# Optimization experiments

Measured on AMD Instinct MI355X. Metric: run time of the kernel, lower is better.

Reference implementation:

```python
import jax, jax.numpy as jnp
import numpy as np

TEMPERATURE = 1.0
# softmax over 32768 db entries gives mean score ~3e-5; threshold 5e-5 makes the
# mask non-trivial (torch default threshold=0.0 would keep everything).
THRESHOLD = 5e-5


def setup_inputs() -> dict:
    key = jax.random.key(0)
    kq, kd = jax.random.split(key)
    queries = jax.random.normal(kq, (8192, 512), dtype=jnp.float32)
    db = jax.random.normal(kd, (32768, 512), dtype=jnp.float32)
    return {"queries": queries, "db": db, "k": 20}


def reference(queries, db, k):
    # similarity matmul: [Nq, Ndb]
    sim_mat = (queries @ db.T) / TEMPERATURE
    # torch does .float().softmax(dim=1)
    all_scores = jax.nn.softmax(sim_mat.astype(jnp.float32), axis=1)
    # db is provided explicitly -> mask_diag = False; k = min(k, db_size)
    k = min(k, db.shape[0])
    topk_scores, topk_inds = jax.lax.top_k(all_scores, k)  # sorted=True
    mask = topk_scores > THRESHOLD
    n_retrieved_per_query = mask.sum(axis=1)
    # padded equivalent of the nonzero-gather: below-threshold slots zeroed
    retrieved_scores = jnp.where(mask, topk_scores, 0.0)
    return retrieved_scores, topk_inds, n_retrieved_per_query, mask
```

## Files before the change

### kernel.cpp

```cpp
#include <hip/hip_runtime.h>
#include <hip/hip_bf16.h>
#include <float.h>
#include <limits.h>

#define NQ 8192
#define ND 32768
#define KD 512
#define TOPK 20
#define NCAND 32
#define NS 16
#define SLICE 2048
#define SEMIT 24
#define EBASE 64.0f
#define ALPHA 2.75f
#define NT (SLICE / 128 * 8)

typedef _Float16 f16x8 __attribute__((ext_vector_type(8)));
typedef _Float16 f16x4 __attribute__((ext_vector_type(4)));
typedef __fp16   hp16x2 __attribute__((ext_vector_type(2)));
typedef float    f32x4 __attribute__((ext_vector_type(4)));

#define CSW(a, b) { unsigned mx_ = (a) > (b) ? (a) : (b); \
                    unsigned mn_ = (a) > (b) ? (b) : (a); (a) = mx_; (b) = mn_; }

__device__ __forceinline__ float fexp64(float q) {
  return __builtin_amdgcn_exp2f(__builtin_fmaf(q, 1.44269504f,
                                               -EBASE * 1.44269504f));
}

__global__ __launch_bounds__(256) void tohalf(
    const float* __restrict__ src, _Float16* __restrict__ dst, int n4)
{
  int g = blockIdx.x * 256 + threadIdx.x;
  if (g >= n4) return;
  float4 v = ((const float4*)src)[g];
  f16x4 h = {(_Float16)v.x, (_Float16)v.y, (_Float16)v.z, (_Float16)v.w};
  ((f16x4*)dst)[g] = h;
}

__device__ __forceinline__ void gload16(const _Float16* g, _Float16* l) {
  __builtin_amdgcn_global_load_lds(
      (const __attribute__((address_space(1))) unsigned int*)g,
      (__attribute__((address_space(3))) unsigned int*)l, 16, 0, 0);
}

#define INSL(x) if ((x) > L7) { L7 = (x); \
  CSW(L6, L7); CSW(L5, L6); CSW(L4, L5); CSW(L3, L4); \
  CSW(L2, L3); CSW(L1, L2); CSW(L0, L1); }
#define INSM(x) if ((x) > M7) { M7 = (x); \
  CSW(M6, M7); CSW(M5, M6); CSW(M4, M5); CSW(M3, M4); \
  CSW(M2, M3); CSW(M1, M2); CSW(M0, M1); }

#define EPIPAIR(va, vb, c0, ES, INS, T) { \
  if (fmaxf((va), (vb)) > (T)) { \
    hp16x2 hp_ = __builtin_amdgcn_cvt_pkrtz((va), (vb)); \
    unsigned pk_ = __builtin_bit_cast(unsigned, hp_); \
    ES += fexp64((float)hp_[0]); \
    ES += fexp64((float)hp_[1]); \
    unsigned sg_ = (pk_ >> 15) & 0x10001u; \
    unsigned u2_ = pk_ ^ (0x80008000u ^ (sg_ * 0x7FFFu)); \
    unsigned k0_ = (u2_ << 16) | (unsigned)(c0); \
    unsigned k1_ = (u2_ & 0xFFFF0000u) | (unsigned)((c0) - 1); \
    INS(k0_); INS(k1_); } }

__global__ __launch_bounds__(256, 2) void fusedsel(
    const _Float16* __restrict__ Qh, const _Float16* __restrict__ Dh,
    unsigned* __restrict__ scand, float* __restrict__ ssum)
{
  __shared__ _Float16 Bs[3][128 * 64];

  const int t = threadIdx.x;
  const int w = t >> 6, l = t & 63;
  const int m0 = blockIdx.x * 128;
  const int ns = blockIdx.y;
  const int lane_mn = l & 15, quad = l >> 4;
  const int row0 = m0 + w * 32 + lane_mn;
  const int row1 = row0 + 16;

  const int sRowIn = l >> 3;
  const int sq = (l & 7) ^ (sRowIn & 7);
  const int fs0 = quad ^ (lane_mn & 7);
  const int fs1 = fs0 ^ 4;

  f16x8 af0[16], af1[16];
  #pragma unroll
  for (int i = 0; i < 16; i++) {
    af0[i] = *(const f16x8*)(Qh + (size_t)row0 * KD + i * 32 + quad * 8);
    af1[i] = *(const f16x8*)(Qh + (size_t)row1 * KD + i * 32 + quad * 8);
  }

  #pragma unroll
  for (int j = 0; j < 4; j++)
    gload16(Dh + (size_t)(ns * SLICE + w * 8 + j * 32 + sRowIn) * KD + sq * 8,
            &Bs[0][(w * 8 + j * 32) * 64]);
  #pragma unroll
  for (int j = 0; j < 4; j++)
    gload16(Dh + (size_t)(ns * SLICE + w * 8 + j * 32 + sRowIn) * KD + 64 + sq * 8,
            &Bs[1][(w * 8 + j * 32) * 64]);

  float nq0 = 0.f, nq1 = 0.f;
  #pragma unroll
  for (int i = 0; i < 16; i++) {
    #pragma unroll
    for (int e = 0; e < 8; e++) {
      float a0 = (float)af0[i][e], a1 = (float)af1[i][e];
      nq0 = __builtin_fmaf(a0, a0, nq0);
      nq1 = __builtin_fmaf(a1, a1, nq1);
    }
  }
  nq0 += __shfl_xor(nq0, 16); nq0 += __shfl_xor(nq0, 32);
  nq1 += __shfl_xor(nq1, 16); nq1 += __shfl_xor(nq1, 32);
  const float T0 = ALPHA * __builtin_sqrtf(nq0);
  const float T1 = ALPHA * __builtin_sqrtf(nq1);

  unsigned L0=0,L1=0,L2=0,L3=0,L4=0,L5=0,L6=0,L7=0;
  unsigned M0=0,M1=0,M2=0,M3=0,M4=0,M5=0,M6=0,M7=0;
  float es0 = 0.f, es1 = 0.f;

  asm volatile("s_waitcnt vmcnt(4)" ::: "memory");
  __builtin_amdgcn_s_barrier();
  int cur = 0;

  for (int ni = 0; ni < SLICE / 128; ni++) {
    const int n0 = ns * SLICE + ni * 128;
    f32x4 acc0[8], acc1[8];
    #pragma unroll
    for (int i = 0; i < 8; i++) {
      acc0[i] = (f32x4){0.f, 0.f, 0.f, 0.f};
      acc1[i] = (f32x4){0.f, 0.f, 0.f, 0.f};
    }

    #pragma unroll
    for (int kk = 0; kk < 8; kk++) {
      const int tt = ni * 8 + kk;

      if (tt + 2 < NT) {
        const int u = tt + 2;
        const int niu = u >> 3, kku = u & 7;
        const int nu = ns * SLICE + niu * 128;
        int nxt = cur + 2; if (nxt >= 3) nxt -= 3;
        _Float16* bsW = &Bs[nxt][0];
        #pragma unroll
        for (int j = 0; j < 4; j++)
          gload16(Dh + (size_t)(nu + w * 8 + j * 32 + sRowIn) * KD + kku * 64 + sq * 8,
                  bsW + (w * 8 + j * 32) * 64);
      }

      const _Float16* bsR = &Bs[cur][0];
      __builtin_amdgcn_s_setprio(1);
      #pragma unroll
      for (int jj = 0; jj < 2; jj++) {
        const int fs = jj ? fs1 : fs0;
        #pragma unroll
        for (int mt = 0; mt < 8; mt++) {
          f16x8 db = *(const f16x8*)&bsR[(mt * 16 + lane_mn) * 64 + fs * 8];
          acc0[mt] = __builtin_amdgcn_mfma_f32_16x16x32_f16(
              db, af0[2 * kk + jj], acc0[mt], 0, 0, 0);
          acc1[mt] = __builtin_amdgcn_mfma_f32_16x16x32_f16(
              db, af1[2 * kk + jj], acc1[mt], 0, 0, 0);
        }
      }
      __builtin_amdgcn_s_setprio(0);

      if (tt < NT - 2) {
        asm volatile("s_waitcnt vmcnt(4)" ::: "memory");
      } else {
        asm volatile("s_waitcnt vmcnt(0)" ::: "memory");
      }
      __builtin_amdgcn_s_barrier();
      cur = (cur == 2) ? 0 : cur + 1;
    }

    const int cb = 0x7FFF - n0 - quad * 4;
    #pragma unroll
    for (int mt = 0; mt < 8; mt++) {
      const int c0 = cb - mt * 16;
      EPIPAIR(acc0[mt][0], acc0[mt][1], c0,     es0, INSL, T0);
      EPIPAIR(acc0[mt][2], acc0[mt][3], c0 - 2, es0, INSL, T0);
      EPIPAIR(acc1[mt][0], acc1[mt][1], c0,     es1, INSM, T1);
      EPIPAIR(acc1[mt][2], acc1[mt][3], c0 - 2, es1, INSM, T1);
    }
  }

  es0 += __shfl_xor(es0, 16); es0 += __shfl_xor(es0, 32);
  es1 += __shfl_xor(es1, 16); es1 += __shfl_xor(es1, 32);
  if (quad == 0) {
    ssum[(size_t)row0 * NS + ns] = es0;
    ssum[(size_t)row1 * NS + ns] = es1;
  }

  for (int s = 0; s < SEMIT; s++) {
    unsigned bk = L0;
    unsigned o = __shfl_xor(bk, 16); bk = bk > o ? bk : o;
    o = __shfl_xor(bk, 32);          bk = bk > o ? bk : o;
    if (L0 == bk) { L0=L1; L1=L2; L2=L3; L3=L4; L4=L5; L5=L6; L6=L7; L7=0; }
    if (quad == 0) scand[(size_t)row0 * (NS * SEMIT) + ns * SEMIT + s] = bk;
  }
  for (int s = 0; s < SEMIT; s++) {
    unsigned bk = M0;
    unsigned o = __shfl_xor(bk, 16); bk = bk > o ? bk : o;
    o = __shfl_xor(bk, 32);          bk = bk > o ? bk : o;
    if (M0 == bk) { M0=M1; M1=M2; M2=M3; M3=M4; M4=M5; M5=M6; M6=M7; M7=0; }
    if (quad == 0) scand[(size_t)row1 * (NS * SEMIT) + ns * SEMIT + s] = bk;
  }
}

__global__ __launch_bounds__(256) void mergecand(
    const unsigned* __restrict__ scand, const float* __restrict__ ssum,
    float* __restrict__ cand_aval, int* __restrict__ cand_idx,
    float* __restrict__ mz)
{
  const int row = blockIdx.x * 4 + (threadIdx.x >> 6);
  const int l = threadIdx.x & 63;
  const unsigned* rk = scand + (size_t)row * (NS * SEMIT);

  unsigned M0=0,M1=0,M2=0,M3=0,M4=0,M5=0;
  #pragma unroll
  for (int j = 0; j < 6; j++) {
    unsigned k = rk[l * 6 + j];
    if (k > M5) {
      M5 = k;
      CSW(M4, M5); CSW(M3, M4); CSW(M2, M3); CSW(M1, M2); CSW(M0, M1);
    }
  }

  float za = (l < NS) ? ssum[(size_t)row * NS + l] : 0.f;
  #pragma unroll
  for (int off = 32; off > 0; off >>= 1) za += __shfl_xor(za, off);

  for (int s = 0; s < NCAND; s++) {
    unsigned bk = M0;
    #pragma unroll
    for (int off = 32; off > 0; off >>= 1) {
      unsigned o = __shfl_xor(bk, off); bk = bk > o ? bk : o;
    }
    if (M0 == bk) { M0=M1; M1=M2; M2=M3; M3=M4; M4=M5; M5=0; }
    if (l == 0) {
      unsigned u = bk >> 16;
      unsigned bs = (u >= 0x8000u) ? (u ^ 0x8000u) : (u ^ 0xFFFFu);
      _Float16 hv = __builtin_bit_cast(_Float16, (unsigned short)bs);
      cand_aval[(size_t)row * NCAND + s] = (float)hv;
      cand_idx [(size_t)row * NCAND + s] = 0x7FFF - (int)(bk & 0x7FFFu);
    }
  }
  if (l == 0) {
    mz[(size_t)row * 2 + 0] = EBASE;
    mz[(size_t)row * 2 + 1] = za;
  }
}

__global__ __launch_bounds__(256) void rescore(
    const float* __restrict__ Q, const float* __restrict__ DB,
    const int* __restrict__ cand_idx, float* __restrict__ exact)
{
  __shared__ float dbS[256][65];
  __shared__ float qS[8][64];
  __shared__ int idxS[256];
  const int t = threadIdx.x;
  const int row0g = blockIdx.x * 8;
  idxS[t] = cand_idx[(size_t)row0g * NCAND + t];
  const int myrow = t >> 5;
  const int sc4 = t >> 2;
  const int sf = t & 3;
  float acc = 0.f;

  for (int k0 = 0; k0 < KD; k0 += 64) {
    __syncthreads();
    #pragma unroll
    for (int cb = 0; cb < 4; cb++) {
      int c = cb * 64 + sc4;
      const float* dp = DB + (size_t)idxS[c] * KD + k0 + sf * 4;
      #pragma unroll
      for (int j = 0; j < 4; j++) {
        float4 v = *(const float4*)(dp + j * 16);
        int e = sf * 4 + j * 16;
        dbS[c][e] = v.x; dbS[c][e + 1] = v.y;
        dbS[c][e + 2] = v.z; dbS[c][e + 3] = v.w;
      }
    }
    if (t < 128) {
      int qr = t >> 4, fi = t & 15;
      float4 v = *(const float4*)(Q + (size_t)(row0g + qr) * KD + k0 + fi * 4);
      *(float4*)&qS[qr][fi * 4] = v;
    }
    __syncthreads();
    #pragma unroll 8
    for (int e = 0; e < 64; e++)
      acc = fmaf(qS[myrow][e], dbS[t][e], acc);
  }
  exact[(size_t)row0g * NCAND + t] = acc;
}

__global__ __launch_bounds__(256) void finalize(
    const float* __restrict__ exact, const float* __restrict__ cand_aval,
    const int* __restrict__ cand_idx, const float* __restrict__ mz,
    float* __restrict__ out)
{
  const int row = blockIdx.x * 4 + (threadIdx.x >> 6);
  const int l = threadIdx.x & 63;
  const bool real = (l < NCAND);

  float e  = real ? exact[(size_t)row * NCAND + l] : -FLT_MAX;
  float av = real ? cand_aval[(size_t)row * NCAND + l] : -FLT_MAX;
  int  idx = real ? cand_idx[(size_t)row * NCAND + l] : INT_MAX;
  const float Ma = mz[(size_t)row * 2 + 0];
  const float Za = mz[(size_t)row * 2 + 1];

  float Me = e;
  #pragma unroll
  for (int off = 32; off > 0; off >>= 1) Me = fmaxf(Me, __shfl_xor(Me, off));

  float ce = real ? __expf(e - Me) : 0.f;
  float ca = real ? __expf(av - Ma) : 0.f;
  float Se = ce, Sa = ca;
  #pragma unroll
  for (int off = 32; off > 0; off >>= 1) {
    Se += __shfl_xor(Se, off);
    Sa += __shfl_xor(Sa, off);
  }
  float Ta = Za - Sa; if (Ta < 0.f) Ta = 0.f;
  const float Ze = Se + Ta * __expf(Ma - Me);

  int rank = 0;
  for (int j = 0; j < NCAND; j++) {
    float ej = __shfl(e, j);
    int   ij = __shfl(idx, j);
    rank += ((ej > e) || (ej == e && ij < idx)) ? 1 : 0;
  }

  const size_t oS = 0;
  const size_t oI = (size_t)NQ * TOPK;
  const size_t oN = (size_t)2 * NQ * TOPK;
  const size_t oM = (size_t)2 * NQ * TOPK + NQ;

  const bool write = real && (rank < TOPK);
  float sc = ce / Ze;
  bool msk = write && ((double)sc > 5e-5);
  if (write) {
    out[oS + (size_t)row * TOPK + rank] = msk ? sc : 0.f;
    out[oI + (size_t)row * TOPK + rank] = (float)idx;
    out[oM + (size_t)row * TOPK + rank] = msk ? 1.f : 0.f;
  }
  unsigned long long bal = __ballot(msk);
  if (l == 0) out[oN + row] = (float)__popcll(bal);
}

extern "C" void kernel_launch(void* const* d_in, const int* in_sizes, int n_in,
                              void* d_out, int out_size, void* d_ws, size_t ws_size,
                              hipStream_t stream) {
  const float* queries = (const float*)d_in[0];
  const float* db      = (const float*)d_in[1];
  float* out = (float*)d_out;

  char* base = (char*)d_ws;
  unsigned* scandP = (unsigned*)base;
  float* ssumP = (float*)(scandP + (size_t)NQ * NS * SEMIT);
  float* exactP = ssumP + (size_t)NQ * NS;
  float* avalP  = exactP + (size_t)NQ * NCAND;
  int*   idxP   = (int*)(avalP + (size_t)NQ * NCAND);
  float* mzP    = (float*)(idxP + (size_t)NQ * NCAND);
  _Float16* Qh  = (_Float16*)(mzP + (size_t)NQ * 2);
  _Float16* Dh  = Qh + (size_t)NQ * KD;

  const int n4q = NQ * KD / 4, n4d = ND * KD / 4;
  tohalf<<<n4q / 256, 256, 0, stream>>>(queries, Qh, n4q);
  tohalf<<<n4d / 256, 256, 0, stream>>>(db, Dh, n4d);

  fusedsel<<<dim3(NQ / 128, NS), 256, 0, stream>>>(Qh, Dh, scandP, ssumP);
  mergecand<<<NQ / 4, 256, 0, stream>>>(scandP, ssumP, avalP, idxP, mzP);
  rescore<<<NQ / 8, 256, 0, stream>>>(queries, db, idxP, exactP);
  finalize<<<NQ / 4, 256, 0, stream>>>(exactP, avalP, idxP, mzP, out);
}
```

Baseline: 510.1 us.

## Fuse candidate merge, exact rescore and finalize into one tail kernel

Merges the two fp32-to-fp16 conversion launches into one kernel. It also fuses mergecand, rescore and finalize into a single tail kernel that keeps candidate indices, approximate values and softmax stats in shared memory instead of round-tripping them through global memory. The finalize logic is remapped so each 32-lane half-wave handles one row, with rank shuffles offset by the half and the ballot split per half. This removes three launches and intermediate global traffic, but the merge phase now runs serially before rescore within each block.

After: 504.2 us. Within noise of the previous version (-1.2%).

```diff
diff --git a/kernel.cpp b/kernel.cpp
--- a/kernel.cpp
+++ b/kernel.cpp
@@ -28,14 +28,22 @@
                                                -EBASE * 1.44269504f));
 }
 
-__global__ __launch_bounds__(256) void tohalf(
-    const float* __restrict__ src, _Float16* __restrict__ dst, int n4)
+__global__ __launch_bounds__(256) void tohalf2(
+    const float* __restrict__ q, const float* __restrict__ d,
+    _Float16* __restrict__ Qh, _Float16* __restrict__ Dh)
 {
+  const int n4q = NQ * KD / 4;
   int g = blockIdx.x * 256 + threadIdx.x;
-  if (g >= n4) return;
-  float4 v = ((const float4*)src)[g];
-  f16x4 h = {(_Float16)v.x, (_Float16)v.y, (_Float16)v.z, (_Float16)v.w};
-  ((f16x4*)dst)[g] = h;
+  if (g < n4q) {
+    float4 v = ((const float4*)q)[g];
+    f16x4 h = {(_Float16)v.x, (_Float16)v.y, (_Float16)v.z, (_Float16)v.w};
+    ((f16x4*)Qh)[g] = h;
+  } else {
+    int gd = g - n4q;
+    float4 v = ((const float4*)d)[gd];
+    f16x4 h = {(_Float16)v.x, (_Float16)v.y, (_Float16)v.z, (_Float16)v.w};
+    ((f16x4*)Dh)[gd] = h;
+  }
 }
 
 __device__ __forceinline__ void gload16(const _Float16* g, _Float16* l) {
@@ -205,60 +213,63 @@
   }
 }
 
-__global__ __launch_bounds__(256) void mergecand(
+__global__ __launch_bounds__(256) void tailk(
     const unsigned* __restrict__ scand, const float* __restrict__ ssum,
-    float* __restrict__ cand_aval, int* __restrict__ cand_idx,
-    float* __restrict__ mz)
-{
-  const int row = blockIdx.x * 4 + (threadIdx.x >> 6);
-  const int l = threadIdx.x & 63;
-  const unsigned* rk = scand + (size_t)row * (NS * SEMIT);
-
-  unsigned M0=0,M1=0,M2=0,M3=0,M4=0,M5=0;
-  #pragma unroll
-  for (int j = 0; j < 6; j++) {
-    unsigned k = rk[l * 6 + j];
-    if (k > M5) {
-      M5 = k;
-      CSW(M4, M5); CSW(M3, M4); CSW(M2, M3); CSW(M1, M2); CSW(M0, M1);
-    }
-  }
-
-  float za = (l < NS) ? ssum[(size_t)row * NS + l] : 0.f;
-  #pragma unroll
-  for (int off = 32; off > 0; off >>= 1) za += __shfl_xor(za, off);
-
-  for (int s = 0; s < NCAND; s++) {
-    unsigned bk = M0;
-    #pragma unroll
-    for (int off = 32; off > 0; off >>= 1) {
-      unsigned o = __shfl_xor(bk, off); bk = bk > o ? bk : o;
-    }
-    if (M0 == bk) { M0=M1; M1=M2; M2=M3; M3=M4; M4=M5; M5=0; }
-    if (l == 0) {
-      unsigned u = bk >> 16;
-      unsigned bs = (u >= 0x8000u) ? (u ^ 0x8000u) : (u ^ 0xFFFFu);
-      _Float16 hv = __builtin_bit_cast(_Float16, (unsigned short)bs);
-      cand_aval[(size_t)row * NCAND + s] = (float)hv;
-      cand_idx [(size_t)row * NCAND + s] = 0x7FFF - (int)(bk & 0x7FFFu);
-    }
-  }
-  if (l == 0) {
-    mz[(size_t)row * 2 + 0] = EBASE;
-    mz[(size_t)row * 2 + 1] = za;
-  }
-}
-
-__global__ __launch_bounds__(256) void rescore(
     const float* __restrict__ Q, const float* __restrict__ DB,
-    const int* __restrict__ cand_idx, float* __restrict__ exact)
+    float* __restrict__ out)
 {
   __shared__ float dbS[256][65];
   __shared__ float qS[8][64];
-  __shared__ int idxS[256];
+  __shared__ int   idxS[256];
+  __shared__ float avalS[256];
+  __shared__ float mzS[8][2];
+
   const int t = threadIdx.x;
+  const int w64 = t >> 6;
+  const int l   = t & 63;
   const int row0g = blockIdx.x * 8;
-  idxS[t] = cand_idx[(size_t)row0g * NCAND + t];
+
+  for (int rr = 0; rr < 2; rr++) {
+    const int br = w64 + rr * 4;
+    const int row = row0g + br;
+    const unsigned* rk = scand + (size_t)row * (NS * SEMIT);
+
+    unsigned M0=0,M1=0,M2=0,M3=0,M4=0,M5=0;
+    #pragma unroll
+    for (int j = 0; j < 6; j++) {
+      unsigned k = rk[l * 6 + j];
+      if (k > M5) {
+        M5 = k;
+        CSW(M4, M5); CSW(M3, M4); CSW(M2, M3); CSW(M1, M2); CSW(M0, M1);
+      }
+    }
+
+    float za = (l < NS) ? ssum[(size_t)row * NS + l] : 0.f;
+    #pragma unroll
+    for (int off = 32; off > 0; off >>= 1) za += __shfl_xor(za, off);
+
+    for (int s = 0; s < NCAND; s++) {
+      unsigned bk = M0;
+      #pragma unroll
+      for (int off = 32; off > 0; off >>= 1) {
+        unsigned o = __shfl_xor(bk, off); bk = bk > o ? bk : o;
+      }
+      if (M0 == bk) { M0=M1; M1=M2; M2=M3; M3=M4; M4=M5; M5=0; }
+      if (l == 0) {
+        unsigned u = bk >> 16;
+        unsigned bs = (u >= 0x8000u) ? (u ^ 0x8000u) : (u ^ 0xFFFFu);
+        _Float16 hv = __builtin_bit_cast(_Float16, (unsigned short)bs);
+        avalS[br * NCAND + s] = (float)hv;
+        idxS [br * NCAND + s] = 0x7FFF - (int)(bk & 0x7FFFu);
+      }
+    }
+    if (l == 0) {
+      mzS[br][0] = EBASE;
+      mzS[br][1] = za;
+    }
+  }
+  __syncthreads();
+
   const int myrow = t >> 5;
   const int sc4 = t >> 2;
   const int sf = t & 3;
@@ -288,33 +299,26 @@
     for (int e = 0; e < 64; e++)
       acc = fmaf(qS[myrow][e], dbS[t][e], acc);
   }
-  exact[(size_t)row0g * NCAND + t] = acc;
-}
-
-__global__ __launch_bounds__(256) void finalize(
-    const float* __restrict__ exact, const float* __restrict__ cand_aval,
-    const int* __restrict__ cand_idx, const float* __restrict__ mz,
-    float* __restrict__ out)
-{
-  const int row = blockIdx.x * 4 + (threadIdx.x >> 6);
-  const int l = threadIdx.x & 63;
-  const bool real = (l < NCAND);
-
-  float e  = real ? exact[(size_t)row * NCAND + l] : -FLT_MAX;
-  float av = real ? cand_aval[(size_t)row * NCAND + l] : -FLT_MAX;
-  int  idx = real ? cand_idx[(size_t)row * NCAND + l] : INT_MAX;
-  const float Ma = mz[(size_t)row * 2 + 0];
-  const float Za = mz[(size_t)row * 2 + 1];
+
+  const int frow = t >> 5;
+  const int fl = t & 31;
+  const int hi = t & 32;
+
+  float e  = acc;
+  float av = avalS[t];
+  int  idx = idxS[t];
+  const float Ma = mzS[frow][0];
+  const float Za = mzS[frow][1];
 
   float Me = e;
   #pragma unroll
-  for (int off = 32; off > 0; off >>= 1) Me = fmaxf(Me, __shfl_xor(Me, off));
-
-  float ce = real ? __expf(e - Me) : 0.f;
-  float ca = real ? __expf(av - Ma) : 0.f;
+  for (int off = 16; off > 0; off >>= 1) Me = fmaxf(Me, __shfl_xor(Me, off));
+
+  float ce = __expf(e - Me);
+  float ca = __expf(av - Ma);
   float Se = ce, Sa = ca;
   #pragma unroll
-  for (int off = 32; off > 0; off >>= 1) {
+  for (int off = 16; off > 0; off >>= 1) {
     Se += __shfl_xor(Se, off);
     Sa += __shfl_xor(Sa, off);
   }
@@ -323,8 +327,8 @@
 
   int rank = 0;
   for (int j = 0; j < NCAND; j++) {
-    float ej = __shfl(e, j);
-    int   ij = __shfl(idx, j);
+    float ej = __shfl(e, hi | j);
+    int   ij = __shfl(idx, hi | j);
     rank += ((ej > e) || (ej == e && ij < idx)) ? 1 : 0;
   }
 
@@ -332,8 +336,9 @@
   const size_t oI = (size_t)NQ * TOPK;
   const size_t oN = (size_t)2 * NQ * TOPK;
   const size_t oM = (size_t)2 * NQ * TOPK + NQ;
-
-  const bool write = real && (rank < TOPK);
+  const int row = row0g + frow;
+
+  const bool write = (rank < TOPK);
   float sc = ce / Ze;
   bool msk = write && ((double)sc > 5e-5);
   if (write) {
@@ -342,7 +347,8 @@
     out[oM + (size_t)row * TOPK + rank] = msk ? 1.f : 0.f;
   }
   unsigned long long bal = __ballot(msk);
-  if (l == 0) out[oN + row] = (float)__popcll(bal);
+  unsigned myhalf = (unsigned)(bal >> hi);
+  if (fl == 0) out[oN + row] = (float)__popc(myhalf);
 }
 
 extern "C" void kernel_launch(void* const* d_in, const int* in_sizes, int n_in,
@@ -361,13 +367,10 @@
   float* mzP    = (float*)(idxP + (size_t)NQ * NCAND);
   _Float16* Qh  = (_Float16*)(mzP + (size_t)NQ * 2);
   _Float16* Dh  = Qh + (size_t)NQ * KD;
+  (void)exactP; (void)avalP; (void)idxP; (void)mzP;
 
   const int n4q = NQ * KD / 4, n4d = ND * KD / 4;
-  tohalf<<<n4q / 256, 256, 0, stream>>>(queries, Qh, n4q);
-  tohalf<<<n4d / 256, 256, 0, stream>>>(db, Dh, n4d);
-
+  tohalf2<<<(n4q + n4d) / 256, 256, 0, stream>>>(queries, db, Qh, Dh);
   fusedsel<<<dim3(NQ / 128, NS), 256, 0, stream>>>(Qh, Dh, scandP, ssumP);
-  mergecand<<<NQ / 4, 256, 0, stream>>>(scandP, ssumP, avalP, idxP, mzP);
-  rescore<<<NQ / 8, 256, 0, stream>>>(queries, db, idxP, exactP);
-  finalize<<<NQ / 4, 256, 0, stream>>>(exactP, avalP, idxP, mzP, out);
-}
+  tailk<<<NQ / 8, 256, 0, stream>>>(scandP, ssumP, queries, db, out);
+}
```
